# Performance work log

Measured on AMD Instinct MI355X. Metric: run time of the kernel, lower is better.

Reference implementation:

```python
import jax, jax.numpy as jnp
import numpy as np

HEADS = 4
DIM_HEAD = 32
SCALE = 16.0
EPS = 1e-5  # jax.nn.standardize default


def _standardize(t):
    # standardize over last axis (the flattened x*y*z sequence), per (b, h, d)
    mu = jnp.mean(t, axis=-1, keepdims=True)
    var = jnp.var(t, axis=-1, keepdims=True)
    return (t - mu) * jax.lax.rsqrt(var + EPS)


def setup_inputs() -> dict:
    key = jax.random.key(0)
    k1, k2, k3 = jax.random.split(key, 3)
    dim = 64
    hidden = HEADS * DIM_HEAD  # 128
    b, x, y, z = 2, 16, 16, 16
    inp = jax.random.normal(k1, (b, x, y, z, dim), dtype=jnp.float32)
    # 1x1x1 convs == pointwise channel matmuls; init like flax lecun_normal-ish scale
    w_qkv = jax.random.normal(k2, (dim, 3 * hidden), dtype=jnp.float32) / np.sqrt(dim)
    w_out = jax.random.normal(k3, (hidden, dim), dtype=jnp.float32) / np.sqrt(hidden)
    b_out = jnp.zeros((dim,), dtype=jnp.float32)
    return {"input": inp, "w_qkv": w_qkv, "w_out": w_out, "b_out": b_out}


def reference(input, w_qkv, w_out, b_out):
    b, x, y, z, c = input.shape
    s = x * y * z
    # pointwise conv -> qkv
    qkv = jnp.einsum('bxyzc,cd->bxyzd', input, w_qkv)  # [b,x,y,z,3*hidden]
    q, k, v = jnp.split(qkv, 3, axis=-1)
    # rearrange 'b x y z (h c) -> b h c (x y z)'
    def to_bhds(t):
        return t.reshape(b, s, HEADS, DIM_HEAD).transpose(0, 2, 3, 1)  # [b,h,d,s]
    q, k, v = map(to_bhds, (q, k, v))
    q = _standardize(q)
    k = _standardize(k)
    sim = jnp.einsum('bhdi,bhdj->bhij', q, k) * SCALE  # [b,h,s,s]
    attn = jax.nn.softmax(sim, axis=-1)
    out = jnp.einsum('bhij,bhdj->bhid', attn, v)  # [b,h,s,d]
    # rearrange 'b h (x y z) d -> b x y z (h d)'
    out = out.transpose(0, 2, 1, 3).reshape(b, x, y, z, HEADS * DIM_HEAD)
    return jnp.einsum('bxyzc,co->bxyzo', out, w_out) + b_out
```

## Files before the change

kernel.cpp:

```cpp
#include <hip/hip_runtime.h>
#include <math.h>
#include <stdint.h>


typedef __attribute__((ext_vector_type(8))) short short8;
typedef __attribute__((ext_vector_type(4))) float f32x4;
typedef __attribute__((ext_vector_type(16))) float f32x16;

#define QSCALE 23.083120654223414f

#if __has_builtin(__builtin_amdgcn_exp2f)
#define EXP2F(x) __builtin_amdgcn_exp2f(x)
#else
#define EXP2F(x) exp2f(x)
#endif

__device__ inline uint32_t pack_hilo(float y) {
  uint32_t uy = __float_as_uint(y);
  uint32_t hb = (uy + 0x7fffu + ((uy >> 16) & 1u)) >> 16;
  float hf = __uint_as_float(hb << 16);
  float r = y - hf;
  uint32_t ur = __float_as_uint(r);
  uint32_t lb = (ur + 0x7fffu + ((ur >> 16) & 1u)) >> 16;
  return (hb << 16) | (lb & 0xffffu);
}

__device__ inline ushort f32_to_bf16(float y) {
  uint32_t uy = __float_as_uint(y);
  return (ushort)((uy + 0x7fffu + ((uy >> 16) & 1u)) >> 16);
}

__device__ inline float bpermf(int addr, float v) {
  return __int_as_float(__builtin_amdgcn_ds_bpermute(addr, __float_as_int(v)));
}

__device__ inline short8 as_s8(uint4 v) {
  union { uint4 u; short8 s; } t;
  t.u = v;
  return t.s;
}

__global__ __launch_bounds__(256) void qkv_kernel(const float* __restrict__ in,
                                                  const float* __restrict__ w,
                                                  float* __restrict__ qf,
                                                  float* __restrict__ kf,
                                                  ushort* __restrict__ vfr,
                                                  float* __restrict__ psum,
                                                  float* __restrict__ psq) {
  __shared__ float As[64][68];
  __shared__ float Bs[64][68];
  __shared__ float ssum[64], ssq[64];
  const int ctile = blockIdx.x % 6;
  const int stile = blockIdx.x / 6;
  const int tid = threadIdx.x;
  const int row0 = stile * 64;
  const int sel = ctile >> 1;

  if (tid < 64) { ssum[tid] = 0.f; ssq[tid] = 0.f; }
  for (int idx = tid; idx < 64 * 64; idx += 256) {
    int s = idx >> 6, c = idx & 63;
    As[s][c] = in[(size_t)(row0 + s) * 64 + c];
  }
  for (int idx = tid; idx < 64 * 64; idx += 256) {
    int c = idx >> 6, ch = idx & 63;
    Bs[c][ch] = w[(size_t)c * 384 + ctile * 64 + ch];
  }
  __syncthreads();

  const int ts = tid >> 4, tc = tid & 15;
  float acc[4][4] = {};
  for (int c = 0; c < 64; c += 4) {
    float4 av[4];
#pragma unroll
    for (int a = 0; a < 4; ++a) av[a] = *(const float4*)&As[ts * 4 + a][c];
    const float4 b0 = *(const float4*)&Bs[c + 0][tc * 4];
    const float4 b1 = *(const float4*)&Bs[c + 1][tc * 4];
    const float4 b2 = *(const float4*)&Bs[c + 2][tc * 4];
    const float4 b3 = *(const float4*)&Bs[c + 3][tc * 4];
    const float bm[4][4] = {{b0.x, b0.y, b0.z, b0.w},
                            {b1.x, b1.y, b1.z, b1.w},
                            {b2.x, b2.y, b2.z, b2.w},
                            {b3.x, b3.y, b3.z, b3.w}};
#pragma unroll
    for (int a = 0; a < 4; ++a) {
      const float aw[4] = {av[a].x, av[a].y, av[a].z, av[a].w};
#pragma unroll
      for (int j = 0; j < 4; ++j)
#pragma unroll
        for (int cc = 0; cc < 4; ++cc) acc[a][cc] = fmaf(aw[j], bm[j][cc], acc[a][cc]);
    }
  }

  const int b = row0 >> 12;
  const int sl = (row0 & 4095) + ts * 4;
  const int chg0 = ctile * 64 + tc * 4;

  if (sel < 2) {
    const int hd0 = chg0 & 127;
    const int h = hd0 >> 5, d0 = hd0 & 31;
    float* dst = (sel == 0 ? qf : kf) + ((size_t)(b * 4 + h) * 4096) * 32 + d0;
#pragma unroll
    for (int a = 0; a < 4; ++a) {
      float4 st = make_float4(acc[a][0], acc[a][1], acc[a][2], acc[a][3]);
      *(float4*)&dst[(size_t)(sl + a) * 32] = st;
    }
#pragma unroll
    for (int cc = 0; cc < 4; ++cc) {
      float sm = acc[0][cc] + acc[1][cc] + acc[2][cc] + acc[3][cc];
      float sq = acc[0][cc] * acc[0][cc] + acc[1][cc] * acc[1][cc] +
                 acc[2][cc] * acc[2][cc] + acc[3][cc] * acc[3][cc];
      atomicAdd(&ssum[tc * 4 + cc], sm);
      atomicAdd(&ssq[tc * 4 + cc], sq);
    }
    __syncthreads();
    if (tid < 64) {
      const int ch = (ctile & 1) * 64 + tid;
      const int idx = (((sel * 2 + b) * 128) + ch) * 64 + (stile & 63);
      psum[idx] = ssum[tid];
      psq[idx] = ssq[tid];
    }
  } else {
    __syncthreads();
    float* VT = &As[0][0];
#pragma unroll
    for (int cc = 0; cc < 4; ++cc)
      *(float4*)&VT[(tc * 4 + cc) * 68 + ts * 4] =
          make_float4(acc[0][cc], acc[1][cc], acc[2][cc], acc[3][cc]);
    __syncthreads();
    const int jt0 = (row0 & 4095) >> 5;
#pragma unroll
    for (int hl = 0; hl < 2; ++hl) {
      const int jtl = tid >> 7, c = (tid >> 6) & 1, ln = tid & 63;
      const int d = ln & 31, hh = ln >> 5;
      const int jloc = 32 * jtl + 16 * c + 8 * hh;
      const int ch = hl * 32 + d;
      const float4 f0 = *(const float4*)&VT[ch * 68 + jloc];
      const float4 f1 = *(const float4*)&VT[ch * 68 + jloc + 4];
      uint4 pk;
      pk.x = (uint32_t)f32_to_bf16(f0.x) | ((uint32_t)f32_to_bf16(f0.y) << 16);
      pk.y = (uint32_t)f32_to_bf16(f0.z) | ((uint32_t)f32_to_bf16(f0.w) << 16);
      pk.z = (uint32_t)f32_to_bf16(f1.x) | ((uint32_t)f32_to_bf16(f1.y) << 16);
      pk.w = (uint32_t)f32_to_bf16(f1.z) | ((uint32_t)f32_to_bf16(f1.w) << 16);
      const int h = (ctile - 4) * 2 + hl;
      ushort* dst =
          vfr + (((size_t)((b * 4 + h) * 128 + jt0 + jtl) * 2 + c) * 64 + ln) * 8;
      *(uint4*)dst = pk;
    }
  }
}

__global__ __launch_bounds__(256) void norm_kernel(const float* __restrict__ qf,
                                                   const float* __restrict__ kf,
                                                   ushort* __restrict__ qfr_hi,
                                                   ushort* __restrict__ qfr_lo,
                                                   ushort* __restrict__ kfr_hi,
                                                   ushort* __restrict__ kfr_lo,
                                                   const float* __restrict__ psum,
                                                   const float* __restrict__ psq) {
  const int bx = blockIdx.x;
  const int tensor = bx >> 7;
  const int bh = (bx >> 4) & 7;
  const int s0 = (bx & 15) * 256;
  const int tid = threadIdx.x;
  __shared__ float red[2][32][8];
  __shared__ float tA[32], tB[32];
  {
    const int d = tid >> 3, p = tid & 7;
    const int base = ((tensor * 2 + (bh >> 2)) * 128 + (bh & 3) * 32 + d) * 64 + p * 8;
    float sm = 0.f, sq = 0.f;
#pragma unroll
    for (int e = 0; e < 8; ++e) {
      sm += psum[base + e];
      sq += psq[base + e];
    }
    red[0][d][p] = sm;
    red[1][d][p] = sq;
  }
  __syncthreads();
  if (tid < 32) {
    float sm = 0.f, sq = 0.f;
#pragma unroll
    for (int e = 0; e < 8; ++e) {
      sm += red[0][tid][e];
      sq += red[1][tid][e];
    }
    const float mu = sm * (1.f / 4096.f);
    const float scale = tensor == 0 ? QSCALE : 1.0f;
    const float inv = rsqrtf(sq * (1.f / 4096.f) - mu * mu + 1e-5f) * scale;
    tA[tid] = inv;
    tB[tid] = -mu * inv;
  }
  __syncthreads();

  const float* src = (tensor == 0 ? qf : kf) + (size_t)bh * 4096 * 32;
  ushort* dhi = (tensor == 0 ? qfr_hi : kfr_hi) + (size_t)(bh * 128 + (s0 >> 5)) * 1024;
  ushort* dlo = (tensor == 0 ? qfr_lo : kfr_lo) + (size_t)(bh * 128 + (s0 >> 5)) * 1024;
#pragma unroll
  for (int pass = 0; pass < 4; ++pass) {
    const int idx = tid + pass * 256;
    const int jtl = idx >> 7;
    const int c = (idx >> 6) & 1;
    const int ln = idx & 63;
    const int p = ln & 31, hh = ln >> 5;
    const int row = tensor == 0 ? p : ((p & 0x13) | ((p & 4) << 1) | ((p & 8) >> 1));
    const int s = s0 + 32 * jtl + row;
    const int d0 = 16 * c + 8 * hh;
    const float4 x0 = *(const float4*)&src[(size_t)s * 32 + d0];
    const float4 x1 = *(const float4*)&src[(size_t)s * 32 + d0 + 4];
    const float4 A0 = *(const float4*)&tA[d0];
    const float4 A1 = *(const float4*)&tA[d0 + 4];
    const float4 B0 = *(const float4*)&tB[d0];
    const float4 B1 = *(const float4*)&tB[d0 + 4];
    uint32_t pk[8];
    pk[0] = pack_hilo(fmaf(x0.x, A0.x, B0.x));
    pk[1] = pack_hilo(fmaf(x0.y, A0.y, B0.y));
    pk[2] = pack_hilo(fmaf(x0.z, A0.z, B0.z));
    pk[3] = pack_hilo(fmaf(x0.w, A0.w, B0.w));
    pk[4] = pack_hilo(fmaf(x1.x, A1.x, B1.x));
    pk[5] = pack_hilo(fmaf(x1.y, A1.y, B1.y));
    pk[6] = pack_hilo(fmaf(x1.z, A1.z, B1.z));
    pk[7] = pack_hilo(fmaf(x1.w, A1.w, B1.w));
    uint4 HV, LV;
    HV.x = __builtin_amdgcn_perm(pk[1], pk[0], 0x07060302u);
    HV.y = __builtin_amdgcn_perm(pk[3], pk[2], 0x07060302u);
    HV.z = __builtin_amdgcn_perm(pk[5], pk[4], 0x07060302u);
    HV.w = __builtin_amdgcn_perm(pk[7], pk[6], 0x07060302u);
    LV.x = __builtin_amdgcn_perm(pk[1], pk[0], 0x05040100u);
    LV.y = __builtin_amdgcn_perm(pk[3], pk[2], 0x05040100u);
    LV.z = __builtin_amdgcn_perm(pk[5], pk[4], 0x05040100u);
    LV.w = __builtin_amdgcn_perm(pk[7], pk[6], 0x05040100u);
    const size_t doff = ((size_t)(jtl * 2 + c) * 64 + ln) * 8;
    *(uint4*)(dhi + doff) = HV;
    *(uint4*)(dlo + doff) = LV;
  }
}

__global__ __launch_bounds__(512, 4) void attn_kernel(const ushort* __restrict__ qfr_hi,
                                                      const ushort* __restrict__ qfr_lo,
                                                      const ushort* __restrict__ kfr_hi,
                                                      const ushort* __restrict__ kfr_lo,
                                                      const ushort* __restrict__ vfr,
                                                      float* __restrict__ o) {
  __shared__ float OM[8 * 32 * 36];
  __shared__ float ML[8 * 64];

  const int tid = threadIdx.x;
  const int w = tid >> 6;
  const int js = w & 3;
  const int itl = w >> 2;
  const int lane = tid & 63;
  const int pl = lane & 31, h2 = lane >> 5;
  const int bh = blockIdx.x & 7;
  const int itp = blockIdx.x >> 3;
  const int it = itp * 2 + itl;

  const size_t qbase = (size_t)(bh * 128 + it) * 1024 + lane * 8;
  const short8 qh0 = *(const short8*)(qfr_hi + qbase);
  const short8 qh1 = *(const short8*)(qfr_hi + qbase + 512);
  const short8 ql0 = *(const short8*)(qfr_lo + qbase);
  const short8 ql1 = *(const short8*)(qfr_lo + qbase + 512);

  const int bp32 = (lane ^ 32) << 2;

  const size_t kbase = (size_t)(bh * 128 + js * 32) * 1024 + lane * 8;
  const ushort* kh = kfr_hi + kbase;
  const ushort* kl = kfr_lo + kbase;
  const ushort* vp = vfr + kbase;

  f32x16 oacc;
#pragma unroll
  for (int r = 0; r < 16; ++r) oacc[r] = 0.f;
  const f32x16 zf = {};
  float m = -INFINITY, l = 0.f;

  uint4 rk0 = *(const uint4*)(kh);
  uint4 rk1 = *(const uint4*)(kh + 512);
  uint4 rl0 = *(const uint4*)(kl);
  uint4 rl1 = *(const uint4*)(kl + 512);
  uint4 rv0 = *(const uint4*)(vp);
  uint4 rv1 = *(const uint4*)(vp + 512);

  for (int t = 0; t < 32; ++t) {
    const short8 ck0 = as_s8(rk0), ck1 = as_s8(rk1);
    const short8 cl0 = as_s8(rl0), cl1 = as_s8(rl1);
    const short8 cv0 = as_s8(rv0), cv1 = as_s8(rv1);
    {
      const int off = (t + 1) * 1024;
      rk0 = *(const uint4*)(kh + off);
      rk1 = *(const uint4*)(kh + off + 512);
      rl0 = *(const uint4*)(kl + off);
      rl1 = *(const uint4*)(kl + off + 512);
      rv0 = *(const uint4*)(vp + off);
      rv1 = *(const uint4*)(vp + off + 512);
    }

    __builtin_amdgcn_s_setprio(1);
    f32x16 sc = __builtin_amdgcn_mfma_f32_32x32x16_bf16(ck0, qh0, zf, 0, 0, 0);
    sc = __builtin_amdgcn_mfma_f32_32x32x16_bf16(ck1, qh1, sc, 0, 0, 0);
    sc = __builtin_amdgcn_mfma_f32_32x32x16_bf16(ck0, ql0, sc, 0, 0, 0);
    sc = __builtin_amdgcn_mfma_f32_32x32x16_bf16(ck1, ql1, sc, 0, 0, 0);
    sc = __builtin_amdgcn_mfma_f32_32x32x16_bf16(cl0, qh0, sc, 0, 0, 0);
    sc = __builtin_amdgcn_mfma_f32_32x32x16_bf16(cl1, qh1, sc, 0, 0, 0);
    __builtin_amdgcn_s_setprio(0);

    const float x0 = fmaxf(fmaxf(sc[0], sc[1]), sc[2]);
    const float x1 = fmaxf(fmaxf(sc[3], sc[4]), sc[5]);
    const float x2 = fmaxf(fmaxf(sc[6], sc[7]), sc[8]);
    const float x3 = fmaxf(fmaxf(sc[9], sc[10]), sc[11]);
    const float x4 = fmaxf(fmaxf(sc[12], sc[13]), sc[14]);
    float mx = fmaxf(fmaxf(fmaxf(x0, x1), x2), fmaxf(fmaxf(x3, x4), sc[15]));
    mx = fmaxf(mx, bpermf(bp32, mx));
    const float mn = fmaxf(m, mx);
    const float al = EXP2F(m - mn);
    m = mn;
#pragma unroll
    for (int r = 0; r < 16; ++r) sc[r] = EXP2F(sc[r] - mn);
    float rs = 0.f;
#pragma unroll
    for (int r = 0; r < 16; ++r) rs += sc[r];
    rs += bpermf(bp32, rs);
    l = l * al + rs;
#pragma unroll
    for (int r = 0; r < 16; ++r) oacc[r] *= al;

    uint32_t pk[8];
#pragma unroll
    for (int i = 0; i < 8; ++i)
      pk[i] = __builtin_amdgcn_perm(__float_as_uint(sc[2 * i + 1]),
                                    __float_as_uint(sc[2 * i]), 0x07060302u);
    union { uint32_t u4[4]; short8 s8; } p0, p1;
    p0.u4[0] = pk[0]; p0.u4[1] = pk[1]; p0.u4[2] = pk[2]; p0.u4[3] = pk[3];
    p1.u4[0] = pk[4]; p1.u4[1] = pk[5]; p1.u4[2] = pk[6]; p1.u4[3] = pk[7];

    __builtin_amdgcn_s_setprio(1);
    oacc = __builtin_amdgcn_mfma_f32_32x32x16_bf16(cv0, p0.s8, oacc, 0, 0, 0);
    oacc = __builtin_amdgcn_mfma_f32_32x32x16_bf16(cv1, p1.s8, oacc, 0, 0, 0);
    __builtin_amdgcn_s_setprio(0);
  }

  {
    float* om = OM + (size_t)(w * 32 + pl) * 36;
#pragma unroll
    for (int g = 0; g < 4; ++g)
      *(float4*)&om[4 * h2 + 8 * g] =
          make_float4(oacc[4 * g], oacc[4 * g + 1], oacc[4 * g + 2], oacc[4 * g + 3]);
    if (h2 == 0) {
      ML[w * 64 + pl] = m;
      ML[w * 64 + 32 + pl] = l;
    }
  }
  __syncthreads();
  const int b = bh >> 2, h = bh & 3;
#pragma unroll
  for (int pass = 0; pass < 4; ++pass) {
    const int idx = tid + pass * 512;
    const int itl2 = idx >> 10;
    const int i = (idx >> 5) & 31;
    const int d = idx & 31;
    const int wb = itl2 * 4;
    const float m0 = ML[(wb + 0) * 64 + i], m1 = ML[(wb + 1) * 64 + i];
    const float m2 = ML[(wb + 2) * 64 + i], m3 = ML[(wb + 3) * 64 + i];
    const float l0 = ML[(wb + 0) * 64 + 32 + i], l1 = ML[(wb + 1) * 64 + 32 + i];
    const float l2 = ML[(wb + 2) * 64 + 32 + i], l3 = ML[(wb + 3) * 64 + 32 + i];
    const float M = fmaxf(fmaxf(m0, m1), fmaxf(m2, m3));
    const float w0 = EXP2F(m0 - M), w1 = EXP2F(m1 - M);
    const float w2 = EXP2F(m2 - M), w3 = EXP2F(m3 - M);
    const float L = l0 * w0 + l1 * w1 + l2 * w2 + l3 * w3;
    const float val = (OM[((wb + 0) * 32 + i) * 36 + d] * w0 +
                       OM[((wb + 1) * 32 + i) * 36 + d] * w1 +
                       OM[((wb + 2) * 32 + i) * 36 + d] * w2 +
                       OM[((wb + 3) * 32 + i) * 36 + d] * w3) *
                      (1.001953125f / L);
    const int ig = (itp * 2 + itl2) * 32 + i;
    o[((size_t)(b * 4096) + ig) * 128 + h * 32 + d] = val;
  }
}

__global__ __launch_bounds__(256) void proj_kernel(const float* __restrict__ o,
                                                   const float* __restrict__ w,
                                                   const float* __restrict__ bias,
                                                   float* __restrict__ out) {
  __shared__ float wT[64 * 132];
  const int tid = threadIdx.x;
  for (int idx = tid; idx < 8192; idx += 256) {
    const int c = idx >> 6, col = idx & 63;
    const int g = (c >> 2) ^ ((col >> 3) & 7);
    wT[col * 132 + (g << 2) + (c & 3)] = w[idx];
  }
  __syncthreads();
  const int col = tid & 63;
  const int r = blockIdx.x * 8 + ((tid >> 6) << 1);
  const float* r0 = o + (size_t)r * 128;
  const float* r1 = r0 + 128;
  const int wbase = col * 132;
  const int gx = (col >> 3) & 7;
  float a0 = bias[col], a1 = a0;
  for (int c = 0; c < 128; c += 4) {
    const float4 x0 = *(const float4*)&r0[c];
    const float4 x1 = *(const float4*)&r1[c];
    const float4 wv = *(const float4*)&wT[wbase + ((((c >> 2) ^ gx)) << 2)];
    a0 = fmaf(x0.x, wv.x, a0); a0 = fmaf(x0.y, wv.y, a0);
    a0 = fmaf(x0.z, wv.z, a0); a0 = fmaf(x0.w, wv.w, a0);
    a1 = fmaf(x1.x, wv.x, a1); a1 = fmaf(x1.y, wv.y, a1);
    a1 = fmaf(x1.z, wv.z, a1); a1 = fmaf(x1.w, wv.w, a1);
  }
  out[(size_t)r * 64 + col] = a0;
  out[(size_t)(r + 1) * 64 + col] = a1;
}

extern "C" void kernel_launch(void* const* d_in, const int* in_sizes, int n_in,
                              void* d_out, int out_size, void* d_ws, size_t ws_size,
                              hipStream_t stream) {
  const float* input = (const float*)d_in[0];
  const float* w_qkv = (const float*)d_in[1];
  const float* w_out = (const float*)d_in[2];
  const float* b_out = (const float*)d_in[3];

  char* W = (char*)d_ws;
  float* qf = (float*)(W + 0);
  float* kf = (float*)(W + (4u << 20));
  ushort* kfr_hi = (ushort*)(W + (8u << 20));
  ushort* kfr_lo = (ushort*)(W + (10u << 20));
  ushort* vfr = (ushort*)(W + (12u << 20));
  ushort* qfr_hi = (ushort*)(W + (14u << 20));
  ushort* qfr_lo = (ushort*)(W + (16u << 20));
  float* psum = (float*)(W + (18u << 20));
  float* psq = (float*)(W + (18u << 20) + (128u << 10));
  float* ob = qf;
  float* out = (float*)d_out;

  hipLaunchKernelGGL(qkv_kernel, dim3(768), dim3(256), 0, stream, input, w_qkv, qf, kf,
                     vfr, psum, psq);
  hipLaunchKernelGGL(norm_kernel, dim3(256), dim3(256), 0, stream, qf, kf, qfr_hi,
                     qfr_lo, kfr_hi, kfr_lo, psum, psq);
  hipLaunchKernelGGL(attn_kernel, dim3(512), dim3(512), 0, stream, qfr_hi, qfr_lo,
                     kfr_hi, kfr_lo, vfr, ob);
  hipLaunchKernelGGL(proj_kernel, dim3(1024), dim3(256), 0, stream, ob, w_out, b_out, out);
}
```

Measured before the change: 143.0 us.

## Compute QKV projection with split-bf16 MFMA instead of scalar FP32 FMA

Replaces the scalar FP32 register-tiled GEMM in the QKV projection kernel with 32x32x16 bf16 MFMA instructions. It uses a hi/lo bf16 split (three MFMAs per k-block) to keep close to FP32 accuracy. Weights are split into hi/lo bf16 in shared memory, and input rows are loaded directly into registers and split there. The epilogue is remapped to the MFMA accumulator layout, which adds per-element strided stores and a different atomic reduction pattern. The intent is to cut the projection's ALU cost, at the price of extra conversion work and small precision differences.

```diff
diff --git a/kernel.cpp b/kernel.cpp
--- a/kernel.cpp
+++ b/kernel.cpp
@@ -47,9 +47,12 @@
                                                   ushort* __restrict__ vfr,
                                                   float* __restrict__ psum,
                                                   float* __restrict__ psq) {
-  __shared__ float As[64][68];
-  __shared__ float Bs[64][68];
+  __shared__ char smem[18432];
   __shared__ float ssum[64], ssq[64];
+  ushort* Bh = (ushort*)smem;
+  ushort* Bl = (ushort*)(smem + 9216);
+  float* VT = (float*)smem;
+
   const int ctile = blockIdx.x % 6;
   const int stile = blockIdx.x / 6;
   const int tid = threadIdx.x;
@@ -57,61 +60,93 @@
   const int sel = ctile >> 1;
 
   if (tid < 64) { ssum[tid] = 0.f; ssq[tid] = 0.f; }
-  for (int idx = tid; idx < 64 * 64; idx += 256) {
-    int s = idx >> 6, c = idx & 63;
-    As[s][c] = in[(size_t)(row0 + s) * 64 + c];
-  }
-  for (int idx = tid; idx < 64 * 64; idx += 256) {
-    int c = idx >> 6, ch = idx & 63;
-    Bs[c][ch] = w[(size_t)c * 384 + ctile * 64 + ch];
+
+  {
+    const int col = tid & 63;
+    const int k0 = (tid >> 6) * 16;
+    const float* wp = w + (size_t)k0 * 384 + ctile * 64 + col;
+    float xv[16];
+#pragma unroll
+    for (int j = 0; j < 16; ++j) xv[j] = wp[(size_t)j * 384];
+    uint32_t hi[8], lo[8];
+#pragma unroll
+    for (int p = 0; p < 8; ++p) {
+      const uint32_t u0 = __float_as_uint(xv[2 * p]);
+      const uint32_t u1 = __float_as_uint(xv[2 * p + 1]);
+      hi[p] = __builtin_amdgcn_perm(u1, u0, 0x07060302u);
+      const float d0 = xv[2 * p] - __uint_as_float(u0 & 0xffff0000u);
+      const float d1 = xv[2 * p + 1] - __uint_as_float(u1 & 0xffff0000u);
+      lo[p] = __builtin_amdgcn_perm(__float_as_uint(d1), __float_as_uint(d0), 0x07060302u);
+    }
+    uint4* bh = (uint4*)&Bh[col * 72 + k0];
+    bh[0] = make_uint4(hi[0], hi[1], hi[2], hi[3]);
+    bh[1] = make_uint4(hi[4], hi[5], hi[6], hi[7]);
+    uint4* bl = (uint4*)&Bl[col * 72 + k0];
+    bl[0] = make_uint4(lo[0], lo[1], lo[2], lo[3]);
+    bl[1] = make_uint4(lo[4], lo[5], lo[6], lo[7]);
   }
   __syncthreads();
 
-  const int ts = tid >> 4, tc = tid & 15;
-  float acc[4][4] = {};
-  for (int c = 0; c < 64; c += 4) {
-    float4 av[4];
-#pragma unroll
-    for (int a = 0; a < 4; ++a) av[a] = *(const float4*)&As[ts * 4 + a][c];
-    const float4 b0 = *(const float4*)&Bs[c + 0][tc * 4];
-    const float4 b1 = *(const float4*)&Bs[c + 1][tc * 4];
-    const float4 b2 = *(const float4*)&Bs[c + 2][tc * 4];
-    const float4 b3 = *(const float4*)&Bs[c + 3][tc * 4];
-    const float bm[4][4] = {{b0.x, b0.y, b0.z, b0.w},
-                            {b1.x, b1.y, b1.z, b1.w},
-                            {b2.x, b2.y, b2.z, b2.w},
-                            {b3.x, b3.y, b3.z, b3.w}};
-#pragma unroll
-    for (int a = 0; a < 4; ++a) {
-      const float aw[4] = {av[a].x, av[a].y, av[a].z, av[a].w};
-#pragma unroll
-      for (int j = 0; j < 4; ++j)
-#pragma unroll
-        for (int cc = 0; cc < 4; ++cc) acc[a][cc] = fmaf(aw[j], bm[j][cc], acc[a][cc]);
-    }
+  const int wv = tid >> 6, lane = tid & 63;
+  const int wr = wv >> 1, wc = wv & 1;
+  const int h2 = lane >> 5, pl = lane & 31;
+
+  short8 ah[4], al[4];
+  {
+    const float* ap = in + (size_t)(row0 + wr * 32 + pl) * 64 + h2 * 8;
+#pragma unroll
+    for (int kb = 0; kb < 4; ++kb) {
+      const float4 xa = *(const float4*)(ap + kb * 16);
+      const float4 xb = *(const float4*)(ap + kb * 16 + 4);
+      const float xs[8] = {xa.x, xa.y, xa.z, xa.w, xb.x, xb.y, xb.z, xb.w};
+      uint32_t hp[4], lp[4];
+#pragma unroll
+      for (int p = 0; p < 4; ++p) {
+        const uint32_t u0 = __float_as_uint(xs[2 * p]);
+        const uint32_t u1 = __float_as_uint(xs[2 * p + 1]);
+        hp[p] = __builtin_amdgcn_perm(u1, u0, 0x07060302u);
+        const float d0 = xs[2 * p] - __uint_as_float(u0 & 0xffff0000u);
+        const float d1 = xs[2 * p + 1] - __uint_as_float(u1 & 0xffff0000u);
+        lp[p] = __builtin_amdgcn_perm(__float_as_uint(d1), __float_as_uint(d0), 0x07060302u);
+      }
+      union { uint32_t u[4]; short8 s; } th, tl;
+      th.u[0] = hp[0]; th.u[1] = hp[1]; th.u[2] = hp[2]; th.u[3] = hp[3];
+      tl.u[0] = lp[0]; tl.u[1] = lp[1]; tl.u[2] = lp[2]; tl.u[3] = lp[3];
+      ah[kb] = th.s;
+      al[kb] = tl.s;
+    }
+  }
+
+  const ushort* bhp = &Bh[(wc * 32 + pl) * 72 + h2 * 8];
+  const ushort* blp = &Bl[(wc * 32 + pl) * 72 + h2 * 8];
+  f32x16 acc = {};
+#pragma unroll
+  for (int kb = 0; kb < 4; ++kb) {
+    const short8 bh = *(const short8*)(bhp + kb * 16);
+    const short8 bl = *(const short8*)(blp + kb * 16);
+    acc = __builtin_amdgcn_mfma_f32_32x32x16_bf16(ah[kb], bh, acc, 0, 0, 0);
+    acc = __builtin_amdgcn_mfma_f32_32x32x16_bf16(ah[kb], bl, acc, 0, 0, 0);
+    acc = __builtin_amdgcn_mfma_f32_32x32x16_bf16(al[kb], bh, acc, 0, 0, 0);
   }
 
   const int b = row0 >> 12;
-  const int sl = (row0 & 4095) + ts * 4;
-  const int chg0 = ctile * 64 + tc * 4;
+  const int sl0 = (row0 & 4095) + wr * 32;
+  const int chg = ctile * 64 + wc * 32 + pl;
 
   if (sel < 2) {
-    const int hd0 = chg0 & 127;
+    const int hd0 = chg & 127;
     const int h = hd0 >> 5, d0 = hd0 & 31;
-    float* dst = (sel == 0 ? qf : kf) + ((size_t)(b * 4 + h) * 4096) * 32 + d0;
-#pragma unroll
-    for (int a = 0; a < 4; ++a) {
-      float4 st = make_float4(acc[a][0], acc[a][1], acc[a][2], acc[a][3]);
-      *(float4*)&dst[(size_t)(sl + a) * 32] = st;
-    }
-#pragma unroll
-    for (int cc = 0; cc < 4; ++cc) {
-      float sm = acc[0][cc] + acc[1][cc] + acc[2][cc] + acc[3][cc];
-      float sq = acc[0][cc] * acc[0][cc] + acc[1][cc] * acc[1][cc] +
-                 acc[2][cc] * acc[2][cc] + acc[3][cc] * acc[3][cc];
-      atomicAdd(&ssum[tc * 4 + cc], sm);
-      atomicAdd(&ssq[tc * 4 + cc], sq);
-    }
+    float* dst = (sel == 0 ? qf : kf) + ((size_t)(b * 4 + h) * 4096 + sl0) * 32 + d0;
+    float s1 = 0.f, s2 = 0.f;
+#pragma unroll
+    for (int reg = 0; reg < 16; ++reg) {
+      const int r = (reg & 3) + 8 * (reg >> 2) + 4 * h2;
+      dst[(size_t)r * 32] = acc[reg];
+      s1 += acc[reg];
+      s2 += acc[reg] * acc[reg];
+    }
+    atomicAdd(&ssum[wc * 32 + pl], s1);
+    atomicAdd(&ssq[wc * 32 + pl], s2);
     __syncthreads();
     if (tid < 64) {
       const int ch = (ctile & 1) * 64 + tid;
@@ -121,11 +156,12 @@
     }
   } else {
     __syncthreads();
-    float* VT = &As[0][0];
-#pragma unroll
-    for (int cc = 0; cc < 4; ++cc)
-      *(float4*)&VT[(tc * 4 + cc) * 68 + ts * 4] =
-          make_float4(acc[0][cc], acc[1][cc], acc[2][cc], acc[3][cc]);
+    const int chv = wc * 32 + pl;
+#pragma unroll
+    for (int reg = 0; reg < 16; ++reg) {
+      const int r = wr * 32 + (reg & 3) + 8 * (reg >> 2) + 4 * h2;
+      VT[chv * 68 + r] = acc[reg];
+    }
     __syncthreads();
     const int jt0 = (row0 & 4095) >> 5;
 #pragma unroll
```

Measured after the change: 131.7 us. -7.9%, faster.
